# Performance work log

Measured on AMD Instinct MI355X. Metric: run time of the kernel, lower is better.

Reference implementation:

```python
import jax, jax.numpy as jnp
import numpy as np

E, TPE, DIM, HID = 64, 128, 1024, 1024  # experts, tokens/expert, model dim, hidden dim
ALPHA = 1.702
LIMIT = 7.0


def setup_inputs() -> dict:
    key = jax.random.key(0)
    k1, k2, k3, k4, k5 = jax.random.split(key, 5)
    std = 0.02
    return {
        "x": jax.random.normal(k1, (E, TPE, DIM), dtype=jnp.float32),
        "mlp1_weight": std * jax.random.normal(k2, (E, DIM, 2 * HID), dtype=jnp.float32),
        "mlp1_bias": std * jax.random.normal(k3, (E, 2 * HID), dtype=jnp.float32),
        "mlp2_weight": std * jax.random.normal(k4, (E, HID, DIM), dtype=jnp.float32),
        "mlp2_bias": std * jax.random.normal(k5, (E, DIM), dtype=jnp.float32),
    }


def _swiglu(h, alpha=ALPHA, limit=LIMIT):
    # interleaved gate/linear split, clamp, sigmoid-gated SwiGLU with +1 on linear path
    x_glu = h[..., 0::2]
    x_lin = h[..., 1::2]
    x_glu = jnp.minimum(x_glu, limit)            # clamp(max=limit), no min
    x_lin = jnp.clip(x_lin, -limit, limit)       # clamp(-limit, limit)
    return x_glu * jax.nn.sigmoid(alpha * x_glu) * (x_lin + 1.0)


def reference(x, mlp1_weight, mlp1_bias, mlp2_weight, mlp2_bias):
    # grouped (per-expert) GEMM 1: [E,T,D] @ [E,D,2H] -> [E,T,2H]
    h = jnp.einsum("etd,edh->eth", x, mlp1_weight) + mlp1_bias[:, None, :]
    h = _swiglu(h)
    # grouped GEMM 2: [E,T,H] @ [E,H,D] -> [E,T,D]
    out = jnp.einsum("eth,ehd->etd", h, mlp2_weight) + mlp2_bias[:, None, :]
    return out
```

## Files before the change

kernel.cpp:

```cpp
#include <hip/hip_runtime.h>
#include <stdint.h>

#define E_  64
#define T_  128
#define D_  1024
#define H_  1024
#define N1_ 2048

typedef __attribute__((ext_vector_type(8))) short bf16x8;
typedef __attribute__((ext_vector_type(4))) float f32x4;

__device__ inline uint32_t pack_bf16(float lo, float hi) {
  union { float f; uint32_t u; } a, b;
  a.f = lo; b.f = hi;
  return __builtin_amdgcn_perm(b.u + 0x8000u, a.u + 0x8000u, 0x07060302u);
}
__device__ inline uint16_t f2bf(float f) {
  union { float f; uint32_t u; } v; v.f = f;
  return (uint16_t)((v.u + 0x8000u) >> 16);
}

#define SA 40

__global__ __launch_bounds__(256) void k1_gemm_swiglu(
    const float* __restrict__ X, const float* __restrict__ W1,
    const float* __restrict__ B1, uint16_t* __restrict__ Act) {
  int blk = blockIdx.x;
  int e  = (blk & 7) + ((blk >> 7) << 3);
  int nt = (blk >> 3) & 15;

  __shared__ uint16_t Asm[128 * SA];
  __shared__ uint16_t Bsm[128 * SA];

  int tid  = threadIdx.x;
  int lane = tid & 63;
  int w    = tid >> 6;
  int wm   = (w & 1) << 6;
  int wn   = (w >> 1) << 6;

  f32x4 acc[4][4];
  #pragma unroll
  for (int i = 0; i < 4; ++i)
    #pragma unroll
    for (int j = 0; j < 4; ++j) { f32x4 z = {0.f,0.f,0.f,0.f}; acc[i][j] = z; }

  const float* Xe  = X  + (size_t)e * T_ * D_;
  const float* W1e = W1 + (size_t)e * D_ * N1_ + nt * 128;

  int a_k4 = tid & 7;
  int a_m  = tid >> 3;
  int b_n  = tid & 127;
  int b_kg = tid >> 7;

  float4 aR[4];
  float  bR[4][4];
  auto load_tiles = [&](int kb) {
    #pragma unroll
    for (int p = 0; p < 4; ++p)
      aR[p] = *(const float4*)(Xe + (size_t)(a_m + 32 * p) * D_ + kb + 4 * a_k4);
    #pragma unroll
    for (int p = 0; p < 4; ++p) {
      const float* src = W1e + (size_t)(kb + 4 * b_kg + 8 * p) * N1_ + b_n;
      bR[p][0] = src[0];
      bR[p][1] = src[N1_];
      bR[p][2] = src[2 * N1_];
      bR[p][3] = src[3 * N1_];
    }
  };

  load_tiles(0);
  #pragma unroll 1
  for (int kt = 0; kt < D_ / 32; ++kt) {
    __syncthreads();
    #pragma unroll
    for (int p = 0; p < 4; ++p) {
      int m = a_m + 32 * p;
      *(uint2*)&Asm[m * SA + 4 * a_k4] =
          make_uint2(pack_bf16(aR[p].x, aR[p].y), pack_bf16(aR[p].z, aR[p].w));
    }
    #pragma unroll
    for (int p = 0; p < 4; ++p) {
      int r = 4 * b_kg + 8 * p;
      *(uint2*)&Bsm[b_n * SA + r] =
          make_uint2(pack_bf16(bR[p][0], bR[p][1]), pack_bf16(bR[p][2], bR[p][3]));
    }
    if (kt < D_ / 32 - 1) load_tiles((kt + 1) * 32);
    __syncthreads();

    bf16x8 af[4], bf[4];
    #pragma unroll
    for (int i = 0; i < 4; ++i) {
      af[i] = *(const bf16x8*)&Asm[(wm + i * 16 + (lane & 15)) * SA + ((lane >> 4) << 3)];
      bf[i] = *(const bf16x8*)&Bsm[(wn + i * 16 + (lane & 15)) * SA + ((lane >> 4) << 3)];
    }
    #pragma unroll
    for (int i = 0; i < 4; ++i)
      #pragma unroll
      for (int j = 0; j < 4; ++j)
        acc[i][j] = __builtin_amdgcn_mfma_f32_16x16x32_bf16(af[i], bf[j], acc[i][j], 0, 0, 0);
  }

  uint16_t* Acte = Act + (size_t)e * T_ * H_;
  #pragma unroll
  for (int j = 0; j < 4; ++j) {
    int col = nt * 128 + wn + j * 16 + (lane & 15);
    float bias = B1[e * N1_ + col];
    #pragma unroll
    for (int i = 0; i < 4; ++i) {
      #pragma unroll
      for (int r = 0; r < 4; ++r) {
        float h = acc[i][j][r] + bias;
        float partner = __shfl_xor(h, 1, 64);
        if ((lane & 1) == 0) {
          float xg = fminf(h, 7.0f);
          float xl = fminf(fmaxf(partner, -7.0f), 7.0f);
          float sw = xg / (1.0f + __expf(-1.702f * xg));
          int m = wm + i * 16 + ((lane >> 4) << 2) + r;
          Acte[m * H_ + (col >> 1)] = f2bf(sw * (xl + 1.0f));
        }
      }
    }
  }
}

__global__ __launch_bounds__(256) void k2_gemm(
    const uint16_t* __restrict__ Act, const float* __restrict__ W2,
    const float* __restrict__ B2, float* __restrict__ OUT) {
  int blk = blockIdx.x;
  int e  = (blk & 7) + ((blk >> 6) << 3);
  int nt = (blk >> 3) & 7;

  __shared__ uint16_t Asm[128 * SA];
  __shared__ uint16_t Bsm[128 * SA];

  int tid  = threadIdx.x;
  int lane = tid & 63;
  int w    = tid >> 6;
  int wm   = (w & 1) << 6;
  int wn   = (w >> 1) << 6;

  f32x4 acc[4][4];
  #pragma unroll
  for (int i = 0; i < 4; ++i)
    #pragma unroll
    for (int j = 0; j < 4; ++j) { f32x4 z = {0.f,0.f,0.f,0.f}; acc[i][j] = z; }

  const uint16_t* Ae  = Act + (size_t)e * T_ * H_;
  const float*    W2e = W2  + (size_t)e * H_ * D_ + nt * 128;

  int a_k2 = tid & 3;
  int a_m  = tid >> 2;
  int b_n  = tid & 127;
  int b_kg = tid >> 7;

  uint4 aR[2];
  float bR[4][4];
  auto load_tiles = [&](int kb) {
    #pragma unroll
    for (int p = 0; p < 2; ++p)
      aR[p] = *(const uint4*)(Ae + (size_t)(a_m + 64 * p) * H_ + kb + 8 * a_k2);
    #pragma unroll
    for (int p = 0; p < 4; ++p) {
      const float* src = W2e + (size_t)(kb + 4 * b_kg + 8 * p) * D_ + b_n;
      bR[p][0] = src[0];
      bR[p][1] = src[D_];
      bR[p][2] = src[2 * D_];
      bR[p][3] = src[3 * D_];
    }
  };

  load_tiles(0);
  #pragma unroll 1
  for (int kt = 0; kt < H_ / 32; ++kt) {
    __syncthreads();
    #pragma unroll
    for (int p = 0; p < 2; ++p)
      *(uint4*)&Asm[(a_m + 64 * p) * SA + 8 * a_k2] = aR[p];
    #pragma unroll
    for (int p = 0; p < 4; ++p) {
      int r = 4 * b_kg + 8 * p;
      *(uint2*)&Bsm[b_n * SA + r] =
          make_uint2(pack_bf16(bR[p][0], bR[p][1]), pack_bf16(bR[p][2], bR[p][3]));
    }
    if (kt < H_ / 32 - 1) load_tiles((kt + 1) * 32);
    __syncthreads();

    bf16x8 af[4], bf[4];
    #pragma unroll
    for (int i = 0; i < 4; ++i) {
      af[i] = *(const bf16x8*)&Asm[(wm + i * 16 + (lane & 15)) * SA + ((lane >> 4) << 3)];
      bf[i] = *(const bf16x8*)&Bsm[(wn + i * 16 + (lane & 15)) * SA + ((lane >> 4) << 3)];
    }
    #pragma unroll
    for (int i = 0; i < 4; ++i)
      #pragma unroll
      for (int j = 0; j < 4; ++j)
        acc[i][j] = __builtin_amdgcn_mfma_f32_16x16x32_bf16(af[i], bf[j], acc[i][j], 0, 0, 0);
  }

  float* Oe = OUT + (size_t)e * T_ * D_;
  #pragma unroll
  for (int j = 0; j < 4; ++j) {
    int col = nt * 128 + wn + j * 16 + (lane & 15);
    float bias = B2[e * D_ + col];
    #pragma unroll
    for (int i = 0; i < 4; ++i) {
      #pragma unroll
      for (int r = 0; r < 4; ++r) {
        int m = wm + i * 16 + ((lane >> 4) << 2) + r;
        Oe[(size_t)m * D_ + col] = acc[i][j][r] + bias;
      }
    }
  }
}

extern "C" void kernel_launch(void* const* d_in, const int* in_sizes, int n_in,
                              void* d_out, int out_size, void* d_ws, size_t ws_size,
                              hipStream_t stream) {
  const float* X  = (const float*)d_in[0];
  const float* W1 = (const float*)d_in[1];
  const float* B1 = (const float*)d_in[2];
  const float* W2 = (const float*)d_in[3];
  const float* B2 = (const float*)d_in[4];
  float* OUT = (float*)d_out;
  uint16_t* Act = (uint16_t*)d_ws;

  k1_gemm_swiglu<<<dim3(E_ * 16), dim3(256), 0, stream>>>(X, W1, B1, Act);
  k2_gemm<<<dim3(E_ * 8), dim3(256), 0, stream>>>(Act, W2, B2, OUT);
}
```

Measured before the change: 894.1 us.

## Restructure LDS layout into k-slabs with vectorized global loads and 16B stores

```diff
diff --git a/kernel.cpp b/kernel.cpp
--- a/kernel.cpp
+++ b/kernel.cpp
@@ -20,17 +20,18 @@
   return (uint16_t)((v.u + 0x8000u) >> 16);
 }
 
-#define SA 40
-
-__global__ __launch_bounds__(256) void k1_gemm_swiglu(
+#define SLAB 1032
+__device__ inline int lds_off(int row, int q) { return q * SLAB + row * 8; }
+
+__global__ __launch_bounds__(256, 3) void k1_gemm_swiglu(
     const float* __restrict__ X, const float* __restrict__ W1,
     const float* __restrict__ B1, uint16_t* __restrict__ Act) {
   int blk = blockIdx.x;
   int e  = (blk & 7) + ((blk >> 7) << 3);
   int nt = (blk >> 3) & 15;
 
-  __shared__ uint16_t Asm[128 * SA];
-  __shared__ uint16_t Bsm[128 * SA];
+  __shared__ uint16_t Asm[4 * SLAB];
+  __shared__ uint16_t Bsm[4 * SLAB];
 
   int tid  = threadIdx.x;
   int lane = tid & 63;
@@ -47,51 +48,55 @@
   const float* Xe  = X  + (size_t)e * T_ * D_;
   const float* W1e = W1 + (size_t)e * D_ * N1_ + nt * 128;
 
-  int a_k4 = tid & 7;
-  int a_m  = tid >> 3;
-  int b_n  = tid & 127;
-  int b_kg = tid >> 7;
+  int a_m  = tid & 127;
+  int a_qh = tid >> 7;
+  int b_c = tid & 63;
+  int b_q = tid >> 6;
 
   float4 aR[4];
-  float  bR[4][4];
+  float2 bR[8];
   auto load_tiles = [&](int kb) {
     #pragma unroll
-    for (int p = 0; p < 4; ++p)
-      aR[p] = *(const float4*)(Xe + (size_t)(a_m + 32 * p) * D_ + kb + 4 * a_k4);
-    #pragma unroll
-    for (int p = 0; p < 4; ++p) {
-      const float* src = W1e + (size_t)(kb + 4 * b_kg + 8 * p) * N1_ + b_n;
-      bR[p][0] = src[0];
-      bR[p][1] = src[N1_];
-      bR[p][2] = src[2 * N1_];
-      bR[p][3] = src[3 * N1_];
-    }
+    for (int c = 0; c < 4; ++c)
+      aR[c] = *(const float4*)(Xe + (size_t)a_m * D_ + kb + 16 * a_qh + 4 * c);
+    #pragma unroll
+    for (int r = 0; r < 8; ++r)
+      bR[r] = *(const float2*)(W1e + (size_t)(kb + 8 * b_q + r) * N1_ + 2 * b_c);
   };
 
   load_tiles(0);
   #pragma unroll 1
   for (int kt = 0; kt < D_ / 32; ++kt) {
     __syncthreads();
-    #pragma unroll
-    for (int p = 0; p < 4; ++p) {
-      int m = a_m + 32 * p;
-      *(uint2*)&Asm[m * SA + 4 * a_k4] =
-          make_uint2(pack_bf16(aR[p].x, aR[p].y), pack_bf16(aR[p].z, aR[p].w));
-    }
-    #pragma unroll
-    for (int p = 0; p < 4; ++p) {
-      int r = 4 * b_kg + 8 * p;
-      *(uint2*)&Bsm[b_n * SA + r] =
-          make_uint2(pack_bf16(bR[p][0], bR[p][1]), pack_bf16(bR[p][2], bR[p][3]));
+    {
+      uint4 w0 = make_uint4(pack_bf16(aR[0].x, aR[0].y), pack_bf16(aR[0].z, aR[0].w),
+                            pack_bf16(aR[1].x, aR[1].y), pack_bf16(aR[1].z, aR[1].w));
+      uint4 w1 = make_uint4(pack_bf16(aR[2].x, aR[2].y), pack_bf16(aR[2].z, aR[2].w),
+                            pack_bf16(aR[3].x, aR[3].y), pack_bf16(aR[3].z, aR[3].w));
+      *(uint4*)&Asm[lds_off(a_m, 2 * a_qh)]     = w0;
+      *(uint4*)&Asm[lds_off(a_m, 2 * a_qh + 1)] = w1;
+    }
+    {
+      uint4 w0 = make_uint4(pack_bf16(bR[0].x, bR[1].x), pack_bf16(bR[2].x, bR[3].x),
+                            pack_bf16(bR[4].x, bR[5].x), pack_bf16(bR[6].x, bR[7].x));
+      uint4 w1 = make_uint4(pack_bf16(bR[0].y, bR[1].y), pack_bf16(bR[2].y, bR[3].y),
+                            pack_bf16(bR[4].y, bR[5].y), pack_bf16(bR[6].y, bR[7].y));
+      *(uint4*)&Bsm[lds_off(b_c,      b_q)] = w0;
+      *(uint4*)&Bsm[lds_off(b_c + 64, b_q)] = w1;
     }
     if (kt < D_ / 32 - 1) load_tiles((kt + 1) * 32);
     __syncthreads();
 
     bf16x8 af[4], bf[4];
-    #pragma unroll
-    for (int i = 0; i < 4; ++i) {
-      af[i] = *(const bf16x8*)&Asm[(wm + i * 16 + (lane & 15)) * SA + ((lane >> 4) << 3)];
-      bf[i] = *(const bf16x8*)&Bsm[(wn + i * 16 + (lane & 15)) * SA + ((lane >> 4) << 3)];
+    int q = lane >> 4;
+    #pragma unroll
+    for (int i = 0; i < 4; ++i)
+      af[i] = *(const bf16x8*)&Asm[lds_off(wm + i * 16 + (lane & 15), q)];
+    #pragma unroll
+    for (int j = 0; j < 4; ++j) {
+      int n = wn + j * 16 + (lane & 15);
+      int rp = (n >> 1) + ((n & 1) << 6);
+      bf[j] = *(const bf16x8*)&Bsm[lds_off(rp, q)];
     }
     #pragma unroll
     for (int i = 0; i < 4; ++i)
@@ -123,15 +128,15 @@
   }
 }
 
-__global__ __launch_bounds__(256) void k2_gemm(
+__global__ __launch_bounds__(256, 3) void k2_gemm(
     const uint16_t* __restrict__ Act, const float* __restrict__ W2,
     const float* __restrict__ B2, float* __restrict__ OUT) {
   int blk = blockIdx.x;
   int e  = (blk & 7) + ((blk >> 6) << 3);
   int nt = (blk >> 3) & 7;
 
-  __shared__ uint16_t Asm[128 * SA];
-  __shared__ uint16_t Bsm[128 * SA];
+  __shared__ uint16_t Asm[4 * SLAB];
+  __shared__ uint16_t Bsm[4 * SLAB];
 
   int tid  = threadIdx.x;
   int lane = tid & 63;
@@ -148,48 +153,49 @@
   const uint16_t* Ae  = Act + (size_t)e * T_ * H_;
   const float*    W2e = W2  + (size_t)e * H_ * D_ + nt * 128;
 
-  int a_k2 = tid & 3;
-  int a_m  = tid >> 2;
-  int b_n  = tid & 127;
-  int b_kg = tid >> 7;
-
-  uint4 aR[2];
-  float bR[4][4];
+  int a_m  = tid & 127;
+  int a_qh = tid >> 7;
+  int b_c = tid & 63;
+  int b_q = tid >> 6;
+
+  uint4  aU[2];
+  float2 bR[8];
   auto load_tiles = [&](int kb) {
     #pragma unroll
-    for (int p = 0; p < 2; ++p)
-      aR[p] = *(const uint4*)(Ae + (size_t)(a_m + 64 * p) * H_ + kb + 8 * a_k2);
-    #pragma unroll
-    for (int p = 0; p < 4; ++p) {
-      const float* src = W2e + (size_t)(kb + 4 * b_kg + 8 * p) * D_ + b_n;
-      bR[p][0] = src[0];
-      bR[p][1] = src[D_];
-      bR[p][2] = src[2 * D_];
-      bR[p][3] = src[3 * D_];
-    }
+    for (int c = 0; c < 2; ++c)
+      aU[c] = *(const uint4*)(Ae + (size_t)a_m * H_ + kb + 16 * a_qh + 8 * c);
+    #pragma unroll
+    for (int r = 0; r < 8; ++r)
+      bR[r] = *(const float2*)(W2e + (size_t)(kb + 8 * b_q + r) * D_ + 2 * b_c);
   };
 
   load_tiles(0);
   #pragma unroll 1
   for (int kt = 0; kt < H_ / 32; ++kt) {
     __syncthreads();
-    #pragma unroll
-    for (int p = 0; p < 2; ++p)
-      *(uint4*)&Asm[(a_m + 64 * p) * SA + 8 * a_k2] = aR[p];
-    #pragma unroll
-    for (int p = 0; p < 4; ++p) {
-      int r = 4 * b_kg + 8 * p;
-      *(uint2*)&Bsm[b_n * SA + r] =
-          make_uint2(pack_bf16(bR[p][0], bR[p][1]), pack_bf16(bR[p][2], bR[p][3]));
+    *(uint4*)&Asm[lds_off(a_m, 2 * a_qh)]     = aU[0];
+    *(uint4*)&Asm[lds_off(a_m, 2 * a_qh + 1)] = aU[1];
+    {
+      uint4 w0 = make_uint4(pack_bf16(bR[0].x, bR[1].x), pack_bf16(bR[2].x, bR[3].x),
+                            pack_bf16(bR[4].x, bR[5].x), pack_bf16(bR[6].x, bR[7].x));
+      uint4 w1 = make_uint4(pack_bf16(bR[0].y, bR[1].y), pack_bf16(bR[2].y, bR[3].y),
+                            pack_bf16(bR[4].y, bR[5].y), pack_bf16(bR[6].y, bR[7].y));
+      *(uint4*)&Bsm[lds_off(b_c,      b_q)] = w0;
+      *(uint4*)&Bsm[lds_off(b_c + 64, b_q)] = w1;
     }
     if (kt < H_ / 32 - 1) load_tiles((kt + 1) * 32);
     __syncthreads();
 
     bf16x8 af[4], bf[4];
-    #pragma unroll
-    for (int i = 0; i < 4; ++i) {
-      af[i] = *(const bf16x8*)&Asm[(wm + i * 16 + (lane & 15)) * SA + ((lane >> 4) << 3)];
-      bf[i] = *(const bf16x8*)&Bsm[(wn + i * 16 + (lane & 15)) * SA + ((lane >> 4) << 3)];
+    int q = lane >> 4;
+    #pragma unroll
+    for (int i = 0; i < 4; ++i)
+      af[i] = *(const bf16x8*)&Asm[lds_off(wm + i * 16 + (lane & 15), q)];
+    #pragma unroll
+    for (int j = 0; j < 4; ++j) {
+      int n = wn + j * 16 + (lane & 15);
+      int rp = (n >> 1) + ((n & 1) << 6);
+      bf[j] = *(const bf16x8*)&Bsm[lds_off(rp, q)];
     }
     #pragma unroll
     for (int i = 0; i < 4; ++i)
```

Result: slower. 935.9 us (+4.7%).
